# Kernel optimization log

Measured on AMD Instinct MI355X. Metric: run time of the kernel, lower is better.

Reference implementation:

```python
import jax, jax.numpy as jnp
import numpy as np

NEG_SLOPE = 0.2
EPS = 1e-16


def gat_conv(x, src, dst, W, a_src, a_dst, bias, heads, out_dim):
    """PyG-style GATConv (add_self_loops already applied via src/dst).
    x: [N, F_in]; src/dst: [E] int; W: [F_in, heads*out_dim];
    a_src/a_dst: [heads, out_dim]; bias: [heads*out_dim] or [out_dim].
    Returns [N, heads*out_dim] (concat) or [N, out_dim] when heads==1.
    """
    N = x.shape[0]
    h = (x @ W).reshape(N, heads, out_dim)                     # [N, H, D]
    alpha_src = jnp.einsum('nhd,hd->nh', h, a_src)             # [N, H]
    alpha_dst = jnp.einsum('nhd,hd->nh', h, a_dst)             # [N, H]
    e = jax.nn.leaky_relu(alpha_src[src] + alpha_dst[dst], NEG_SLOPE)  # [E, H]
    # segment softmax over edges grouped by destination node
    m = jax.ops.segment_max(e, dst, num_segments=N)            # [N, H]
    ex = jnp.exp(e - m[dst])                                   # [E, H]
    s = jax.ops.segment_sum(ex, dst, num_segments=N)           # [N, H]
    alpha = ex / (s[dst] + EPS)                                # [E, H]
    msg = h[src] * alpha[:, :, None]                           # [E, H, D]
    out = jax.ops.segment_sum(msg, dst, num_segments=N)        # [N, H, D]
    return out.reshape(N, heads * out_dim) + bias


def setup_inputs() -> dict:
    key = jax.random.key(0)
    ks = jax.random.split(key, 12)
    N, E = 50000, 1600000
    F_in, H, D, C = 128, 8, 8, 40
    x = jax.random.normal(ks[0], (N, F_in), dtype=jnp.float32)
    edge_index = jax.random.randint(ks[1], (2, E), 0, N, dtype=jnp.int32)
    edge_attr = jax.random.normal(ks[2], (E, 1), dtype=jnp.float32)
    # Glorot-ish init for weights, zeros for bias (PyG defaults)
    W1 = jax.random.normal(ks[3], (F_in, H * D), dtype=jnp.float32) * (1.0 / np.sqrt(F_in))
    att_src1 = jax.random.normal(ks[4], (H, D), dtype=jnp.float32) * (1.0 / np.sqrt(D))
    att_dst1 = jax.random.normal(ks[5], (H, D), dtype=jnp.float32) * (1.0 / np.sqrt(D))
    bias1 = jnp.zeros((H * D,), dtype=jnp.float32)
    W2 = jax.random.normal(ks[6], (H * D, C), dtype=jnp.float32) * (1.0 / np.sqrt(H * D))
    att_src2 = jax.random.normal(ks[7], (1, C), dtype=jnp.float32) * (1.0 / np.sqrt(C))
    att_dst2 = jax.random.normal(ks[8], (1, C), dtype=jnp.float32) * (1.0 / np.sqrt(C))
    bias2 = jnp.zeros((C,), dtype=jnp.float32)
    return {"x": x, "edge_index": edge_index, "edge_attr": edge_attr,
            "W1": W1, "att_src1": att_src1, "att_dst1": att_dst1, "bias1": bias1,
            "W2": W2, "att_src2": att_src2, "att_dst2": att_dst2, "bias2": bias2}


def reference(x, edge_index, edge_attr, W1, att_src1, att_dst1, bias1,
              W2, att_src2, att_dst2, bias2):
    N = x.shape[0]
    x = x.astype(jnp.float32)
    edge_attr = edge_attr.astype(jnp.float32)  # cast as original; unused downstream
    # add self-loops (PyG GATConv default add_self_loops=True)
    loop = jnp.arange(N, dtype=edge_index.dtype)
    src = jnp.concatenate([edge_index[0], loop])
    dst = jnp.concatenate([edge_index[1], loop])
    h = gat_conv(x, src, dst, W1, att_src1, att_dst1, bias1, heads=8, out_dim=8)
    h = jax.nn.elu(h)
    out = gat_conv(h, src, dst, W2, att_src2, att_dst2, bias2, heads=1, out_dim=W2.shape[1])
    return out
```

## Files before the change

kernel.cpp:

```cpp
#include <hip/hip_runtime.h>
#include <hip/hip_fp16.h>
#include <cstdint>

#define NEG_SLOPE 0.2f
#define EPSV 1e-16f

#define BIN_SHIFT 7
#define NODES_PER_BIN 128
#define MAXBINS 512
#define CHUNK 2048

typedef _Float16 half8v __attribute__((ext_vector_type(8)));
typedef float float4v __attribute__((ext_vector_type(4)));
typedef int v4i __attribute__((ext_vector_type(4)));
typedef int v2i __attribute__((ext_vector_type(2)));

__device__ float buf_load_f32(v4i rsrc, int voffset, int soffset, int aux) __asm("llvm.amdgcn.raw.buffer.load.f32");
__device__ int   buf_load_i32(v4i rsrc, int voffset, int soffset, int aux) __asm("llvm.amdgcn.raw.buffer.load.i32");
__device__ v2i   buf_load_2xi32(v4i rsrc, int voffset, int soffset, int aux) __asm("llvm.amdgcn.raw.buffer.load.v2i32");

__device__ inline v4i make_rsrc(const void* p, unsigned bytes) {
    union { v4i v; struct { const void* p; unsigned range; unsigned cfg; } s; } u;
    u.s.p = p; u.s.range = bytes; u.s.cfg = 0x00020000u;
    return u.v;
}

__global__ __launch_bounds__(256) void gemm1_hist(
    const float* __restrict__ x, const float* __restrict__ W1,
    const float* __restrict__ aS, const float* __restrict__ aD,
    __half* __restrict__ h1h, float* __restrict__ as1, float* __restrict__ ad1, int N,
    const int* __restrict__ dsts, int* __restrict__ offmat,
    int E, int Et, int nbins, int nb, int gemmBlocks)
{
    __shared__ _Float16 xh[64 * 128];
    __shared__ _Float16 wt[64 * 128];
    __shared__ int lhist[MAXBINS];
    int t = threadIdx.x;

    if ((int)blockIdx.x >= gemmBlocks) {
        int blk = blockIdx.x - gemmBlocks;
        for (int i = t; i < nbins; i += 256) lhist[i] = 0;
        __syncthreads();
        int base = blk * CHUNK;
#pragma unroll
        for (int r = 0; r < CHUNK / 256; ++r) {
            int i = base + r * 256 + t;
            if (i < Et) {
                int dn = (i < E) ? dsts[i] : (i - E);
                atomicAdd(&lhist[dn >> BIN_SHIFT], 1);
            }
        }
        __syncthreads();
        for (int i = t; i < nbins; i += 256)
            offmat[(size_t)i * nb + blk] = lhist[i];
        return;
    }

    int n0 = blockIdx.x * 64;
    const float2* x2 = (const float2*)x;
#pragma unroll
    for (int i = 0; i < 16; ++i) {
        int p = t + i * 256;
        int n = p >> 6, kp = p & 63;
        int gn = n0 + n;
        float2 v = (gn < N) ? x2[(size_t)gn * 64 + kp] : make_float2(0.f, 0.f);
        union { _Float16 h[2]; uint32_t u; } cv;
        cv.h[0] = (_Float16)v.x; cv.h[1] = (_Float16)v.y;
        *(uint32_t*)&xh[n * 128 + ((kp * 2) ^ ((n & 7) << 3))] = cv.u;
    }
#pragma unroll
    for (int i = 0; i < 32; ++i) {
        int p = t + i * 256;
        int k = p >> 6, c = p & 63;
        wt[c * 128 + (k ^ ((c & 7) << 3))] = (_Float16)W1[p];
    }
    __syncthreads();

    int wv = t >> 6, l = t & 63;
    int m0 = wv * 16;
    int lr = l & 15;
    int lg = l >> 4;
    float4v acc[4];
#pragma unroll
    for (int ct = 0; ct < 4; ++ct) acc[ct] = (float4v)(0.f);
#pragma unroll
    for (int kt = 0; kt < 4; ++kt) {
        int kh0 = kt * 32 + lg * 8;
        int an = m0 + lr;
        half8v aF = *(half8v*)&xh[an * 128 + (kh0 ^ ((an & 7) << 3))];
#pragma unroll
        for (int ct = 0; ct < 4; ++ct) {
            int c = ct * 16 + lr;
            half8v bF = *(half8v*)&wt[c * 128 + (kh0 ^ ((c & 7) << 3))];
            acc[ct] = __builtin_amdgcn_mfma_f32_16x16x32_f16(aF, bF, acc[ct], 0, 0, 0);
        }
    }
#pragma unroll
    for (int ct = 0; ct < 4; ++ct) {
        int c = ct * 16 + lr;
        float asc = aS[c], adc = aD[c];
#pragma unroll
        for (int i = 0; i < 4; ++i) {
            int n = n0 + m0 + lg * 4 + i;
            float v = acc[ct][i];
            float s = v * asc, d = v * adc;
            s += __shfl_xor(s, 1, 64); s += __shfl_xor(s, 2, 64); s += __shfl_xor(s, 4, 64);
            d += __shfl_xor(d, 1, 64); d += __shfl_xor(d, 2, 64); d += __shfl_xor(d, 4, 64);
            if (n < N) {
                h1h[(size_t)n * 64 + c] = __float2half(v);
                if ((l & 7) == 0) {
                    int hd = 2 * ct + ((l >> 3) & 1);
                    as1[n * 8 + hd] = s;
                    ad1[n * 8 + hd] = d;
                }
            }
        }
    }
}

__global__ __launch_bounds__(256) void binscan2(
    int* __restrict__ offmat, int* __restrict__ bincnt, int nb)
{
    __shared__ int tsum[256];
    __shared__ int carry;
    int b = blockIdx.x, t = threadIdx.x;
    int* row = offmat + (size_t)b * nb;
    if (t == 0) carry = 0;
    __syncthreads();
    for (int base = 0; base < nb; base += 1024) {
        int i0 = base + t * 4;
        int v0 = (i0 + 0 < nb) ? row[i0 + 0] : 0;
        int v1 = (i0 + 1 < nb) ? row[i0 + 1] : 0;
        int v2 = (i0 + 2 < nb) ? row[i0 + 2] : 0;
        int v3 = (i0 + 3 < nb) ? row[i0 + 3] : 0;
        int s = v0 + v1 + v2 + v3;
        tsum[t] = s;
        __syncthreads();
        for (int off = 1; off < 256; off <<= 1) {
            int y = (t >= off) ? tsum[t - off] : 0;
            __syncthreads();
            tsum[t] += y;
            __syncthreads();
        }
        int e = tsum[t] - s + carry;
        if (i0 + 0 < nb) row[i0 + 0] = e;        e += v0;
        if (i0 + 1 < nb) row[i0 + 1] = e;        e += v1;
        if (i0 + 2 < nb) row[i0 + 2] = e;        e += v2;
        if (i0 + 3 < nb) row[i0 + 3] = e;
        __syncthreads();
        if (t == 255) carry += tsum[255];
        __syncthreads();
    }
    if (t == 0) bincnt[b] = carry;
}

__global__ __launch_bounds__(256) void binscan(
    const int* __restrict__ bincnt, int* __restrict__ binoff,
    int* __restrict__ row_ptr, int nbins, int N, int Et)
{
    __shared__ int tsum[256];
    int t = threadIdx.x;
    int i0 = t * 2;
    int v0 = (i0 + 0 < nbins) ? bincnt[i0 + 0] : 0;
    int v1 = (i0 + 1 < nbins) ? bincnt[i0 + 1] : 0;
    int s = v0 + v1;
    tsum[t] = s;
    __syncthreads();
    for (int off = 1; off < 256; off <<= 1) {
        int y = (t >= off) ? tsum[t - off] : 0;
        __syncthreads();
        tsum[t] += y;
        __syncthreads();
    }
    int e = tsum[t] - s;
    if (i0 + 0 < nbins) binoff[i0 + 0] = e;  e += v0;
    if (i0 + 1 < nbins) binoff[i0 + 1] = e;
    if (t == 255) binoff[nbins] = tsum[255];
    if (t == 0) row_ptr[N] = Et;
}

__global__ __launch_bounds__(256) void binscatter(
    const int* __restrict__ srcs, const int* __restrict__ dsts,
    const int* __restrict__ binoff, const int* __restrict__ offmat,
    unsigned int* __restrict__ binned, int E, int Et, int nbins, int nb)
{
    __shared__ int gbase[MAXBINS];
    __shared__ int lcur[MAXBINS];
    int t = threadIdx.x, blk = blockIdx.x;
    for (int i = t; i < nbins; i += 256) {
        gbase[i] = binoff[i] + offmat[(size_t)i * nb + blk];
        lcur[i] = 0;
    }
    __syncthreads();
    int base = blk * CHUNK;
#pragma unroll
    for (int r = 0; r < CHUNK / 256; ++r) {
        int i = base + r * 256 + t;
        if (i < Et) {
            int s, dn;
            if (i < E) { s = srcs[i]; dn = dsts[i]; }
            else       { s = i - E;   dn = s; }
            int b = dn >> BIN_SHIFT;
            int li = atomicAdd(&lcur[b], 1);
            binned[gbase[b] + li] = ((unsigned)(dn & (NODES_PER_BIN - 1)) << 24) | (unsigned)s;
        }
    }
}

__global__ __launch_bounds__(256) void binsort(
    const unsigned int* __restrict__ binned, const int* __restrict__ binoff,
    int* __restrict__ row_ptr, int* __restrict__ colx, int N, int nbins)
{
    __shared__ int lh[NODES_PER_BIN];
    __shared__ int lcur[NODES_PER_BIN];
    int b = blockIdx.x, t = threadIdx.x;
    int beg = binoff[b], end = binoff[b + 1];
    if (t < NODES_PER_BIN) lh[t] = 0;
    __syncthreads();
    for (int j = beg + t; j < end; j += 256)
        atomicAdd(&lh[binned[j] >> 24], 1);
    __syncthreads();
    int own = (t < NODES_PER_BIN) ? lh[t] : 0;
    for (int off = 1; off < NODES_PER_BIN; off <<= 1) {
        int y = (t >= off && t < NODES_PER_BIN) ? lh[t - off] : 0;
        __syncthreads();
        if (t < NODES_PER_BIN) lh[t] += y;
        __syncthreads();
    }
    if (t < NODES_PER_BIN) {
        int excl = lh[t] - own;
        int gnode = (b << BIN_SHIFT) + t;
        if (gnode < N) row_ptr[gnode] = beg + excl;
        lcur[t] = excl;
    }
    __syncthreads();
    for (int j = beg + t; j < end; j += 256) {
        unsigned p = binned[j];
        int pos = atomicAdd(&lcur[p >> 24], 1);
        colx[beg + pos] = (int)(p & 0xFFFFFF);
    }
}

__global__ __launch_bounds__(256) void gather1(
    const int* __restrict__ row_ptr, const int* __restrict__ colx,
    const float* __restrict__ as1, const float* __restrict__ ad1,
    const __half* __restrict__ h1h, const float* __restrict__ bias1,
    float* __restrict__ helu, int N)
{
    int wave = (blockIdx.x * 256 + threadIdx.x) >> 6;
    if (wave >= N) return;
    int lane = threadIdx.x & 63;
    int q = lane >> 4;
    int sl = lane & 15;
    int hh = sl >> 1;
    int sl8 = sl << 3;
    v4i rsH = make_rsrc(h1h, (unsigned)N * 128u);
    v4i rsA = make_rsrc(as1, (unsigned)N * 32u);
    int n = wave;
    float adn = ad1[n * 8 + hh];
    int beg = row_ptr[n], end = row_ptr[n + 1];
    float ax = 0.f, ay = 0.f, az = 0.f, aw = 0.f, ws = 0.f;
    int albase = lane >> 3;
    int alhead = (lane & 7) << 2;

    for (int cb = beg; cb < end; cb += 64) {
        int cnt = min(64, end - cb);
        int sv = (cb + lane < end) ? colx[cb + lane] : 0;
        int groups = (cnt + 7) >> 3;
        for (int g = 0; g < groups; ++g) {
            int gk = g << 3;
            int sg = __shfl(sv, gk + albase, 64);
            float aV = buf_load_f32(rsA, (sg << 5) + alhead, 0, 0);
#pragma unroll
            for (int hs = 0; hs < 2; ++hs) {
                int e = (hs << 2) + q;
                int k = gk + e;
                int s = __shfl(sv, k, 64);
                float a = __shfl(aV, (e << 3) + hh, 64);
                v2i hv = buf_load_2xi32(rsH, (s << 7) + sl8, 0, 0);
                float ee = a + adn; ee = fmaxf(ee, NEG_SLOPE * ee);
                float w = (k < cnt) ? __expf(ee) : 0.f;
                union { int i; __half2 h; } u0, u1; u0.i = hv[0]; u1.i = hv[1];
                float2 f0 = __half22float2(u0.h);
                float2 f1 = __half22float2(u1.h);
                ax = fmaf(w, f0.x, ax); ay = fmaf(w, f0.y, ay);
                az = fmaf(w, f1.x, az); aw = fmaf(w, f1.y, aw);
                ws += w;
            }
        }
    }
    ax += __shfl_xor(ax, 16, 64); ax += __shfl_xor(ax, 32, 64);
    ay += __shfl_xor(ay, 16, 64); ay += __shfl_xor(ay, 32, 64);
    az += __shfl_xor(az, 16, 64); az += __shfl_xor(az, 32, 64);
    aw += __shfl_xor(aw, 16, 64); aw += __shfl_xor(aw, 32, 64);
    ws += __shfl_xor(ws, 16, 64); ws += __shfl_xor(ws, 32, 64);
    if (lane < 16) {
        float4 b = ((const float4*)bias1)[sl];
        float inv = 1.f / (ws + EPSV);
        float v0 = ax * inv + b.x;
        float v1 = ay * inv + b.y;
        float v2 = az * inv + b.z;
        float v3 = aw * inv + b.w;
        v0 = (v0 > 0.f) ? v0 : (__expf(v0) - 1.f);
        v1 = (v1 > 0.f) ? v1 : (__expf(v1) - 1.f);
        v2 = (v2 > 0.f) ? v2 : (__expf(v2) - 1.f);
        v3 = (v3 > 0.f) ? v3 : (__expf(v3) - 1.f);
        *(float4*)&helu[(size_t)n * 64 + (sl << 2)] = make_float4(v0, v1, v2, v3);
    }
}

__global__ __launch_bounds__(256) void gemm2_alpha(
    const float* __restrict__ helu, const float* __restrict__ W2,
    const float* __restrict__ aS, const float* __restrict__ aD,
    __half* __restrict__ h2h, float* __restrict__ as2, float* __restrict__ ad2, int N)
{
    __shared__ _Float16 xh[64 * 64];
    __shared__ _Float16 wt[48 * 64];
    int t = threadIdx.x;
    int n0 = blockIdx.x * 64;

    for (int i = t; i < (48 * 64) / 2; i += 256) ((uint32_t*)wt)[i] = 0;
    __syncthreads();

    const float2* h2p = (const float2*)helu;
#pragma unroll
    for (int i = 0; i < 8; ++i) {
        int p = t + i * 256;
        int n = p >> 5, kp = p & 31;
        int gn = n0 + n;
        float2 v = (gn < N) ? h2p[(size_t)gn * 32 + kp] : make_float2(0.f, 0.f);
        union { _Float16 h[2]; uint32_t u; } cv;
        cv.h[0] = (_Float16)v.x; cv.h[1] = (_Float16)v.y;
        *(uint32_t*)&xh[n * 64 + ((kp * 2) ^ ((n & 7) << 3))] = cv.u;
    }
#pragma unroll
    for (int i = 0; i < 10; ++i) {
        int p = t + i * 256;
        if (p < 64 * 40) {
            int k = p / 40, c = p - k * 40;
            wt[c * 64 + (k ^ ((c & 7) << 3))] = (_Float16)W2[p];
        }
    }
    __syncthreads();

    int wv = t >> 6, l = t & 63;
    int m0 = wv * 16;
    int lr = l & 15;
    int lg = l >> 4;
    float4v acc[3];
#pragma unroll
    for (int ct = 0; ct < 3; ++ct) acc[ct] = (float4v)(0.f);
#pragma unroll
    for (int kt = 0; kt < 2; ++kt) {
        int kh0 = kt * 32 + lg * 8;
        int an = m0 + lr;
        half8v aF = *(half8v*)&xh[an * 64 + (kh0 ^ ((an & 7) << 3))];
#pragma unroll
        for (int ct = 0; ct < 3; ++ct) {
            int c = ct * 16 + lr;
            half8v bF = *(half8v*)&wt[c * 64 + (kh0 ^ ((c & 7) << 3))];
            acc[ct] = __builtin_amdgcn_mfma_f32_16x16x32_f16(aF, bF, acc[ct], 0, 0, 0);
        }
    }
    float sv[4] = {0.f, 0.f, 0.f, 0.f};
    float dv[4] = {0.f, 0.f, 0.f, 0.f};
#pragma unroll
    for (int ct = 0; ct < 3; ++ct) {
        int c = ct * 16 + lr;
        bool av = (c < 40);
        float asc = av ? aS[c] : 0.f;
        float adc = av ? aD[c] : 0.f;
#pragma unroll
        for (int i = 0; i < 4; ++i) {
            int n = n0 + m0 + lg * 4 + i;
            float v = acc[ct][i];
            sv[i] = fmaf(v, asc, sv[i]);
            dv[i] = fmaf(v, adc, dv[i]);
            if (av && n < N) h2h[(size_t)n * 64 + c] = __float2half(v);
        }
    }
#pragma unroll
    for (int i = 0; i < 4; ++i) {
        float s = sv[i], d = dv[i];
        s += __shfl_xor(s, 1, 64); s += __shfl_xor(s, 2, 64);
        s += __shfl_xor(s, 4, 64); s += __shfl_xor(s, 8, 64);
        d += __shfl_xor(d, 1, 64); d += __shfl_xor(d, 2, 64);
        d += __shfl_xor(d, 4, 64); d += __shfl_xor(d, 8, 64);
        int n = n0 + m0 + lg * 4 + i;
        if (lr == 0 && n < N) { as2[n] = s; ad2[n] = d; }
    }
}

__global__ __launch_bounds__(256) void gather2(
    const int* __restrict__ row_ptr, const int* __restrict__ colx,
    const float* __restrict__ as2, const float* __restrict__ ad2,
    const __half* __restrict__ h2h, const float* __restrict__ bias2,
    float* __restrict__ out, int N)
{
    int wave = (blockIdx.x * 256 + threadIdx.x) >> 6;
    if (wave >= N) return;
    int lane = threadIdx.x & 63;
    int q = lane >> 4;
    int sl = lane & 15;
    int sl8 = sl << 3;
    v4i rsH = make_rsrc(h2h, (unsigned)N * 128u);
    v4i rsA = make_rsrc(as2, (unsigned)N * 4u);
    int n = wave;
    float adn = ad2[n];
    int beg = row_ptr[n], end = row_ptr[n + 1];
    float ax = 0.f, ay = 0.f, az = 0.f, aw = 0.f, ws = 0.f;

#define G2_BODY(ii) { \
    int k = ((ii) << 2) + q; \
    int s = __shfl(sv, k, 64); \
    float a = __shfl(aV, k, 64); \
    v2i hv = buf_load_2xi32(rsH, (s << 7) + sl8, 0, 0); \
    float ee = a + adn; ee = fmaxf(ee, NEG_SLOPE * ee); \
    float w = (k < cnt) ? __expf(ee) : 0.f; \
    union { int i; __half2 h; } u0, u1; u0.i = hv[0]; u1.i = hv[1]; \
    float2 f0 = __half22float2(u0.h); \
    float2 f1 = __half22float2(u1.h); \
    ax = fmaf(w, f0.x, ax); ay = fmaf(w, f0.y, ay); \
    az = fmaf(w, f1.x, az); aw = fmaf(w, f1.y, aw); \
    ws += w; }

    for (int cb = beg; cb < end; cb += 64) {
        int cnt = min(64, end - cb);
        int sv = (cb + lane < end) ? colx[cb + lane] : 0;
        float aV = buf_load_f32(rsA, sv << 2, 0, 0);
        int iters = (cnt + 3) >> 2;
        int i = 0;
        for (; i + 2 <= iters; i += 2) { G2_BODY(i) G2_BODY(i + 1) }
        for (; i < iters; ++i) { G2_BODY(i) }
    }
#undef G2_BODY

    ax += __shfl_xor(ax, 16, 64); ax += __shfl_xor(ax, 32, 64);
    ay += __shfl_xor(ay, 16, 64); ay += __shfl_xor(ay, 32, 64);
    az += __shfl_xor(az, 16, 64); az += __shfl_xor(az, 32, 64);
    aw += __shfl_xor(aw, 16, 64); aw += __shfl_xor(aw, 32, 64);
    ws += __shfl_xor(ws, 16, 64); ws += __shfl_xor(ws, 32, 64);
    if (lane < 10) {
        float4 b = *(const float4*)&bias2[sl << 2];
        float inv = 1.f / (ws + EPSV);
        *(float4*)&out[(size_t)n * 40 + (sl << 2)] =
            make_float4(ax * inv + b.x, ay * inv + b.y, az * inv + b.z, aw * inv + b.w);
    }
}

extern "C" void kernel_launch(void* const* d_in, const int* in_sizes, int n_in,
                              void* d_out, int out_size, void* d_ws, size_t ws_size,
                              hipStream_t stream)
{
    const float* x   = (const float*)d_in[0];
    const int*   ei  = (const int*)d_in[1];
    const float* W1  = (const float*)d_in[3];
    const float* aS1 = (const float*)d_in[4];
    const float* aD1 = (const float*)d_in[5];
    const float* b1  = (const float*)d_in[6];
    const float* W2  = (const float*)d_in[7];
    const float* aS2 = (const float*)d_in[8];
    const float* aD2 = (const float*)d_in[9];
    const float* b2  = (const float*)d_in[10];

    int N  = in_sizes[0] / 128;
    int E  = in_sizes[1] / 2;
    int Et = E + N;
    int nbins = (N + NODES_PER_BIN - 1) >> BIN_SHIFT;
    int nb = (Et + CHUNK - 1) / CHUNK;

    float* fws   = (float*)d_ws;
    float* as1   = fws;
    float* ad1   = as1  + (size_t)N * 8;
    float* helu  = ad1  + (size_t)N * 8;
    float* as2   = helu + (size_t)N * 64;
    float* ad2   = as2  + (size_t)N;
    __half* h1h  = (__half*)(ad2 + (size_t)N);
    __half* h2h  = h1h + (size_t)N * 64;
    int*   iws     = (int*)(h2h + (size_t)N * 64);
    int*   row_ptr = iws;
    int*   bincnt  = row_ptr + N + 1;
    int*   binoff  = bincnt + MAXBINS + 1;
    int*   offmat  = binoff + MAXBINS + 1;
    unsigned int* binned = (unsigned int*)(offmat + (size_t)MAXBINS * nb);
    int*   colx    = (int*)(binned + Et);
    float* out     = (float*)d_out;

    const int* srcs = ei;
    const int* dsts = ei + E;

    int gemmBlocks = (N + 63) / 64;

    gemm1_hist<<<gemmBlocks + nb, 256, 0, stream>>>(
        x, W1, aS1, aD1, h1h, as1, ad1, N, dsts, offmat, E, Et, nbins, nb, gemmBlocks);

    binscan2<<<nbins, 256, 0, stream>>>(offmat, bincnt, nb);
    binscan<<<1, 256, 0, stream>>>(bincnt, binoff, row_ptr, nbins, N, Et);
    binscatter<<<nb, 256, 0, stream>>>(srcs, dsts, binoff, offmat, binned, E, Et, nbins, nb);
    binsort<<<nbins, 256, 0, stream>>>(binned, binoff, row_ptr, colx, N, nbins);

    gather1<<<(N * 64 + 255) / 256, 256, 0, stream>>>(row_ptr, colx, as1, ad1,
        h1h, b1, helu, N);

    gemm2_alpha<<<(N + 63) / 64, 256, 0, stream>>>(helu, W2, aS2, aD2, h2h, as2, ad2, N);
    gather2<<<(N * 64 + 255) / 256, 256, 0, stream>>>(row_ptr, colx, as2, ad2,
        h2h, b2, out, N);
}
```

Measured before the change: 139.1 us.

## Split layer-1 features into two head-halves and gather each with its own wave

The layer-1 fp16 feature matrix is stored as two planar halves (heads 0-3 and heads 4-7, 32 halfs per node each) instead of interleaved 64-wide rows. gather1 now launches two waves per destination node, one per half, and each wave walks 8 edges per group across 64 lanes. Each half-table is half the size, which is meant to improve cache locality for the random source-row gathers and to double wave-level parallelism. In exchange, the column indices and attention logits are loaded twice per node, and the cross-lane reduction needs an extra shuffle step.

```diff
diff --git a/kernel.cpp b/kernel.cpp
--- a/kernel.cpp
+++ b/kernel.cpp
@@ -99,6 +99,7 @@
     for (int ct = 0; ct < 4; ++ct) {
         int c = ct * 16 + lr;
         float asc = aS[c], adc = aD[c];
+        size_t hbase = (size_t)(c >> 5) * N * 32 + (c & 31);
 #pragma unroll
         for (int i = 0; i < 4; ++i) {
             int n = n0 + m0 + lg * 4 + i;
@@ -107,7 +108,7 @@
             s += __shfl_xor(s, 1, 64); s += __shfl_xor(s, 2, 64); s += __shfl_xor(s, 4, 64);
             d += __shfl_xor(d, 1, 64); d += __shfl_xor(d, 2, 64); d += __shfl_xor(d, 4, 64);
             if (n < N) {
-                h1h[(size_t)n * 64 + c] = __float2half(v);
+                h1h[hbase + (size_t)n * 32] = __float2half(v);
                 if ((l & 7) == 0) {
                     int hd = 2 * ct + ((l >> 3) & 1);
                     as1[n * 8 + hd] = s;
@@ -247,21 +248,20 @@
     const __half* __restrict__ h1h, const float* __restrict__ bias1,
     float* __restrict__ helu, int N)
 {
-    int wave = (blockIdx.x * 256 + threadIdx.x) >> 6;
-    if (wave >= N) return;
+    int w = (blockIdx.x * 256 + threadIdx.x) >> 6;
+    if (w >= 2 * N) return;
+    int p = (w >= N) ? 1 : 0;
+    int n = w - p * N;
     int lane = threadIdx.x & 63;
-    int q = lane >> 4;
-    int sl = lane & 15;
-    int hh = sl >> 1;
-    int sl8 = sl << 3;
-    v4i rsH = make_rsrc(h1h, (unsigned)N * 128u);
+    int o = lane >> 3;
+    int sl = lane & 7;
+    int hh = (p << 2) + (sl >> 1);
+    v4i rsH = make_rsrc(h1h + (size_t)p * N * 32, (unsigned)N * 64u);
     v4i rsA = make_rsrc(as1, (unsigned)N * 32u);
-    int n = wave;
     float adn = ad1[n * 8 + hh];
     int beg = row_ptr[n], end = row_ptr[n + 1];
     float ax = 0.f, ay = 0.f, az = 0.f, aw = 0.f, ws = 0.f;
-    int albase = lane >> 3;
-    int alhead = (lane & 7) << 2;
+    int alhead = sl << 2;
 
     for (int cb = beg; cb < end; cb += 64) {
         int cnt = min(64, end - cb);
@@ -269,33 +269,29 @@
         int groups = (cnt + 7) >> 3;
         for (int g = 0; g < groups; ++g) {
             int gk = g << 3;
-            int sg = __shfl(sv, gk + albase, 64);
+            int sg = __shfl(sv, gk + o, 64);
             float aV = buf_load_f32(rsA, (sg << 5) + alhead, 0, 0);
-#pragma unroll
-            for (int hs = 0; hs < 2; ++hs) {
-                int e = (hs << 2) + q;
-                int k = gk + e;
-                int s = __shfl(sv, k, 64);
-                float a = __shfl(aV, (e << 3) + hh, 64);
-                v2i hv = buf_load_2xi32(rsH, (s << 7) + sl8, 0, 0);
-                float ee = a + adn; ee = fmaxf(ee, NEG_SLOPE * ee);
-                float w = (k < cnt) ? __expf(ee) : 0.f;
-                union { int i; __half2 h; } u0, u1; u0.i = hv[0]; u1.i = hv[1];
-                float2 f0 = __half22float2(u0.h);
-                float2 f1 = __half22float2(u1.h);
-                ax = fmaf(w, f0.x, ax); ay = fmaf(w, f0.y, ay);
-                az = fmaf(w, f1.x, az); aw = fmaf(w, f1.y, aw);
-                ws += w;
-            }
-        }
-    }
-    ax += __shfl_xor(ax, 16, 64); ax += __shfl_xor(ax, 32, 64);
-    ay += __shfl_xor(ay, 16, 64); ay += __shfl_xor(ay, 32, 64);
-    az += __shfl_xor(az, 16, 64); az += __shfl_xor(az, 32, 64);
-    aw += __shfl_xor(aw, 16, 64); aw += __shfl_xor(aw, 32, 64);
-    ws += __shfl_xor(ws, 16, 64); ws += __shfl_xor(ws, 32, 64);
-    if (lane < 16) {
-        float4 b = ((const float4*)bias1)[sl];
+            int k = gk + o;
+            int s = __shfl(sv, k, 64);
+            float a = __shfl(aV, (o << 3) + hh, 64);
+            v2i hv = buf_load_2xi32(rsH, (s << 6) + (sl << 3), 0, 0);
+            float ee = a + adn; ee = fmaxf(ee, NEG_SLOPE * ee);
+            float wgt = (k < cnt) ? __expf(ee) : 0.f;
+            union { int i; __half2 h; } u0, u1; u0.i = hv[0]; u1.i = hv[1];
+            float2 f0 = __half22float2(u0.h);
+            float2 f1 = __half22float2(u1.h);
+            ax = fmaf(wgt, f0.x, ax); ay = fmaf(wgt, f0.y, ay);
+            az = fmaf(wgt, f1.x, az); aw = fmaf(wgt, f1.y, aw);
+            ws += wgt;
+        }
+    }
+    ax += __shfl_xor(ax, 8, 64); ax += __shfl_xor(ax, 16, 64); ax += __shfl_xor(ax, 32, 64);
+    ay += __shfl_xor(ay, 8, 64); ay += __shfl_xor(ay, 16, 64); ay += __shfl_xor(ay, 32, 64);
+    az += __shfl_xor(az, 8, 64); az += __shfl_xor(az, 16, 64); az += __shfl_xor(az, 32, 64);
+    aw += __shfl_xor(aw, 8, 64); aw += __shfl_xor(aw, 16, 64); aw += __shfl_xor(aw, 32, 64);
+    ws += __shfl_xor(ws, 8, 64); ws += __shfl_xor(ws, 16, 64); ws += __shfl_xor(ws, 32, 64);
+    if (lane < 8) {
+        float4 b = *(const float4*)&bias1[p * 32 + (sl << 2)];
         float inv = 1.f / (ws + EPSV);
         float v0 = ax * inv + b.x;
         float v1 = ay * inv + b.y;
@@ -305,7 +301,7 @@
         v1 = (v1 > 0.f) ? v1 : (__expf(v1) - 1.f);
         v2 = (v2 > 0.f) ? v2 : (__expf(v2) - 1.f);
         v3 = (v3 > 0.f) ? v3 : (__expf(v3) - 1.f);
-        *(float4*)&helu[(size_t)n * 64 + (sl << 2)] = make_float4(v0, v1, v2, v3);
+        *(float4*)&helu[(size_t)n * 64 + p * 32 + (sl << 2)] = make_float4(v0, v1, v2, v3);
     }
 }
 
@@ -499,7 +495,7 @@
     binscatter<<<nb, 256, 0, stream>>>(srcs, dsts, binoff, offmat, binned, E, Et, nbins, nb);
     binsort<<<nbins, 256, 0, stream>>>(binned, binoff, row_ptr, colx, N, nbins);
 
-    gather1<<<(N * 64 + 255) / 256, 256, 0, stream>>>(row_ptr, colx, as1, ad1,
+    gather1<<<(2 * N * 64 + 255) / 256, 256, 0, stream>>>(row_ptr, colx, as1, ad1,
         h1h, b1, helu, N);
 
     gemm2_alpha<<<(N + 63) / 64, 256, 0, stream>>>(helu, W2, aS2, aD2, h2h, as2, ad2, N);
```

After: 175.5 us. 1.26x slower.
